# Performance work log

Hardware: AMD Instinct MI355X
Metric: run time of the kernel (lower is better)

Reference implementation:

```python
import jax, jax.numpy as jnp
import numpy as np

DIM = 2048
H = 16       # num_heads
HKV = 4      # num_kv_heads
HD = DIM // H  # head_dim = 128
REP = H // HKV
ROPE_BASE = 10000.0
QK_GAIN_INIT = 1.0
B, T = 4, 2048


def rms_norm(x):
    # F.rms_norm with eps=None -> machine eps of dtype, no weight
    eps = jnp.finfo(x.dtype).eps
    return x * jax.lax.rsqrt(jnp.mean(x * x, axis=-1, keepdims=True) + eps)


def apply_rotary_emb(x, cos, sin):
    # x: [B, h, T, HD]; cos/sin: [T, HD//2]
    h = x.shape[-1] // 2
    x1, x2 = x[..., :h], x[..., h:]
    return jnp.concatenate((x1 * cos + x2 * sin, -x1 * sin + x2 * cos), axis=-1)


def setup_inputs() -> dict:
    key = jax.random.key(0)
    ks = jax.random.split(key, 6)
    kv_dim = HKV * HD
    x = jax.random.normal(ks[0], (B, T, DIM), dtype=jnp.float32)
    Wq = jax.random.normal(ks[1], (DIM, DIM), dtype=jnp.float32) * 0.02
    Wk = jax.random.normal(ks[2], (kv_dim, DIM), dtype=jnp.float32) * 0.02
    Wv = jax.random.normal(ks[3], (kv_dim, DIM), dtype=jnp.float32) * 0.02
    Wproj = jax.random.normal(ks[4], (DIM, DIM), dtype=jnp.float32) * 0.02
    q_gain = jnp.full((H,), QK_GAIN_INIT, dtype=jnp.float32)
    return {"x": x, "Wq": Wq, "Wk": Wk, "Wv": Wv, "Wproj": Wproj, "q_gain": q_gain}


def reference(x, Wq, Wk, Wv, Wproj, q_gain):
    Bs, Ts, D = x.shape
    # QKV projections (bias-free Linear: x @ W.T)
    q = (x @ Wq.T).reshape(Bs, Ts, H, HD).transpose(0, 2, 1, 3)      # [B,H,T,HD]
    k = (x @ Wk.T).reshape(Bs, Ts, HKV, HD).transpose(0, 2, 1, 3)    # [B,HKV,T,HD]
    v = (x @ Wv.T).reshape(Bs, Ts, HKV, HD).transpose(0, 2, 1, 3)
    # RMSNorm over head_dim
    q, k = rms_norm(q), rms_norm(k)
    # rotary
    inv_freq = 1.0 / (ROPE_BASE ** (jnp.arange(0, HD, 2, dtype=jnp.float32) / HD))
    t = jnp.arange(Ts, dtype=jnp.float32)
    freqs = jnp.outer(t, inv_freq)  # [T, HD//2]
    cos, sin = jnp.cos(freqs), jnp.sin(freqs)
    q = apply_rotary_emb(q, cos, sin)
    k = apply_rotary_emb(k, cos, sin)
    # per-head query gain
    q = q * q_gain[None, :, None, None]
    # GQA attention without materializing repeated K/V
    qg = q.reshape(Bs, HKV, REP, Ts, HD)
    scale = 1.0 / jnp.sqrt(jnp.asarray(HD, dtype=q.dtype))
    scores = jnp.einsum('bgrtd,bgsd->bgrts', qg, k) * scale  # [B,HKV,REP,T,T]
    causal = jnp.tril(jnp.ones((Ts, Ts), dtype=bool))
    scores = jnp.where(causal, scores, jnp.finfo(scores.dtype).min)
    attn = jax.nn.softmax(scores, axis=-1)
    y = jnp.einsum('bgrts,bgsd->bgrtd', attn, v)              # [B,HKV,REP,T,HD]
    y = y.reshape(Bs, H, Ts, HD).transpose(0, 2, 1, 3).reshape(Bs, Ts, D)
    return y @ Wproj.T
```

## Files before the change

### kernel.cpp

```cpp
#include <hip/hip_runtime.h>
#include <stdint.h>

typedef unsigned short u16;
typedef __attribute__((ext_vector_type(4))) float f32x4;
typedef __attribute__((ext_vector_type(8))) __bf16 bf16x8;
typedef __attribute__((ext_vector_type(4))) u16 u16x4;
typedef __attribute__((ext_vector_type(8))) u16 u16x8;

#define T_SEQ 2048
#define NB 4
#define NH 16
#define NKV 4
#define HDIM 128
#define PSTR 72

__device__ __forceinline__ u16 f2bf(float f) {
  __bf16 h = (__bf16)f;
  return __builtin_bit_cast(u16, h);
}
__device__ __forceinline__ float bf2f(u16 u) {
  union { uint32_t u; float f; } v; v.u = ((uint32_t)u) << 16;
  return v.f;
}
__device__ __forceinline__ void gload16(const void* g, void* l) {
  __builtin_amdgcn_global_load_lds((const __attribute__((address_space(1))) void*)g,
                                   (__attribute__((address_space(3))) void*)l, 16, 0, 0);
}
__device__ __forceinline__ f32x4 mfma16(bf16x8 a, bf16x8 b, f32x4 c) {
  return __builtin_amdgcn_mfma_f32_16x16x32_bf16(a, b, c, 0, 0, 0);
}

__global__ __launch_bounds__(256) void cvt_all(const float* __restrict__ x,
                                               const float* __restrict__ wq,
                                               const float* __restrict__ wk,
                                               const float* __restrict__ wv,
                                               const float* __restrict__ wp,
                                               u16* __restrict__ xo, u16* __restrict__ wqo,
                                               u16* __restrict__ wko, u16* __restrict__ wvo,
                                               u16* __restrict__ wpo) {
  const int C_X = 16777216 / 4, C_WQ = 4194304 / 4, C_WKV = 1048576 / 4;
  const int B1 = C_X, B2 = B1 + C_WQ, B3 = B2 + C_WKV, B4 = B3 + C_WKV;
  const int total = B4 + C_WQ;
  int idx = blockIdx.x * 256 + threadIdx.x;
  int stride = gridDim.x * 256;
  for (int c = idx; c < total; c += stride) {
    const float* src;
    u16* dst;
    int off;
    if (c < B1)      { src = x;  dst = xo;  off = c; }
    else if (c < B2) { src = wq; dst = wqo; off = c - B1; }
    else if (c < B3) { src = wk; dst = wko; off = c - B2; }
    else if (c < B4) { src = wv; dst = wvo; off = c - B3; }
    else             { src = wp; dst = wpo; off = c - B4; }
    f32x4 v = *(const f32x4*)(src + (size_t)off * 4);
    u16x4 o;
    o[0] = f2bf(v[0]); o[1] = f2bf(v[1]); o[2] = f2bf(v[2]); o[3] = f2bf(v[3]);
    *(u16x4*)(dst + (size_t)off * 4) = o;
  }
}

template <int MODE>
__global__ __launch_bounds__(256) void gemm128p3(const u16* __restrict__ A,
                                                 const u16* __restrict__ Bt,
                                                 u16* __restrict__ k_o, u16* __restrict__ v_o,
                                                 float* __restrict__ f_o,
                                                 int K, int nx, int cpx) {
  __shared__ __align__(16) u16 As3[3 * 128 * 32];
  __shared__ __align__(16) u16 Bs3[3 * 128 * 32];
  const int tid = threadIdx.x;
  const int l = tid & 63, w = tid >> 6;
  const int l15 = l & 15, g16 = l >> 4;
  const int wr = w >> 1, wc = w & 1;

  const int oid = blockIdx.x + nx * blockIdx.y;
  const int wid = (oid & 7) * cpx + (oid >> 3);
  const int m0 = (wid / nx) * 128, n0 = (wid % nx) * 128;

  f32x4 acc[4][4] = {};

  const int row0 = tid >> 2, row1 = 64 + (tid >> 2), cc = tid & 3;
  const int sc0 = cc ^ ((row0 >> 1) & 3), sc1 = cc ^ ((row1 >> 1) & 3);
  const u16* pA0 = A + (size_t)(m0 + row0) * K + sc0 * 8;
  const u16* pA1 = A + (size_t)(m0 + row1) * K + sc1 * 8;
  const u16* pB0 = Bt + (size_t)(n0 + row0) * K + sc0 * 8;
  const u16* pB1 = Bt + (size_t)(n0 + row1) * K + sc1 * 8;

#define STAGE(buf)                                                   \
  {                                                                  \
    char* ab = (char*)As3 + (buf) * 8192 + w * 1024;                 \
    char* bb = (char*)Bs3 + (buf) * 8192 + w * 1024;                 \
    gload16(pA0, ab);                                                \
    gload16(pA1, ab + 4096);                                         \
    gload16(pB0, bb);                                                \
    gload16(pB1, bb + 4096);                                         \
    pA0 += 32; pA1 += 32; pB0 += 32; pB1 += 32;                      \
  }

#define COMPUTE(buf)                                                 \
  {                                                                  \
    const u16* AsB = As3 + (buf) * 4096;                             \
    const u16* BsB = Bs3 + (buf) * 4096;                             \
    bf16x8 af[4], bfr[4];                                            \
    _Pragma("unroll")                                                \
    for (int mt = 0; mt < 4; ++mt) {                                 \
      int arow = wr * 64 + mt * 16 + l15;                            \
      af[mt] = *(const bf16x8*)&AsB[arow * 32 +                      \
                                    ((g16 ^ ((arow >> 1) & 3)) * 8)];\
    }                                                                \
    _Pragma("unroll")                                                \
    for (int nt = 0; nt < 4; ++nt) {                                 \
      int brow = wc * 64 + nt * 16 + l15;                            \
      bfr[nt] = *(const bf16x8*)&BsB[brow * 32 +                     \
                                     ((g16 ^ ((brow >> 1) & 3)) * 8)];\
    }                                                                \
    __builtin_amdgcn_s_setprio(1);                                   \
    _Pragma("unroll")                                                \
    for (int mt = 0; mt < 4; ++mt)                                   \
      _Pragma("unroll")                                              \
      for (int nt = 0; nt < 4; ++nt)                                 \
        acc[mt][nt] = mfma16(af[mt], bfr[nt], acc[mt][nt]);          \
    __builtin_amdgcn_s_setprio(0);                                   \
  }

  const int ntiles = K >> 5;
  STAGE(0);
  STAGE(1);
  asm volatile("s_waitcnt vmcnt(4)" ::: "memory");
  __builtin_amdgcn_s_barrier();

  int cur = 0, nxt = 2;
  for (int t = 0; t < ntiles; ++t) {
    const bool more2 = (t + 2 < ntiles);
    if (more2) STAGE(nxt);
    COMPUTE(cur);
    if (t + 1 < ntiles) {
      if (more2) {
        asm volatile("s_waitcnt vmcnt(4)" ::: "memory");
      } else {
        asm volatile("s_waitcnt vmcnt(0)" ::: "memory");
      }
      __builtin_amdgcn_s_barrier();
    }
    cur = (cur == 2) ? 0 : cur + 1;
    nxt = (nxt == 2) ? 0 : nxt + 1;
  }
#undef STAGE
#undef COMPUTE

#pragma unroll
  for (int mt = 0; mt < 4; ++mt) {
#pragma unroll
    for (int r = 0; r < 4; ++r) {
      int row = m0 + wr * 64 + mt * 16 + g16 * 4 + r;
#pragma unroll
      for (int nt = 0; nt < 4; ++nt) {
        int n = n0 + wc * 64 + nt * 16 + l15;
        float val = acc[mt][nt][r];
        if (MODE == 1) {
          f_o[(size_t)row * 2048 + n] = val;
        } else {
          int b = row >> 11, t = row & (T_SEQ - 1);
          u16 bv = f2bf(val);
          if (n < 512) {
            int h = n >> 7, d = n & 127;
            k_o[((size_t)(b * NKV + h) * T_SEQ + t) * HDIM + d] = bv;
          } else {
            int n2 = n - 512; int h = n2 >> 7, d = n2 & 127;
            v_o[((size_t)(b * NKV + h) * T_SEQ + t) * HDIM + d] = bv;
          }
        }
      }
    }
  }
}

template <int MODE>
__global__ __launch_bounds__(512, 2) void gemm256(const u16* __restrict__ A,
                                                  const u16* __restrict__ Bt,
                                                  u16* __restrict__ q_o,
                                                  float* __restrict__ f_o,
                                                  int K, int ntn, int cpx) {
  __shared__ __align__(16) u16 As[2][256 * 64];
  __shared__ __align__(16) u16 Bs[2][256 * 64];
  const int tid = threadIdx.x;
  const int l = tid & 63, w = tid >> 6;
  const int l16 = l & 15, g16 = l >> 4;
  const int wr = w >> 2, wc = w & 3;

  const int oid = blockIdx.x;
  const int wid = (oid & 7) * cpx + (oid >> 3);
  const int m0 = (wid / ntn) * 256, n0 = (wid % ntn) * 256;

  f32x4 acc[8][4] = {};

  const int srow = tid >> 3, scc = tid & 7;
  const u16* pA[4];
  const u16* pB[4];
#pragma unroll
  for (int j = 0; j < 4; ++j) {
    int row = j * 64 + srow;
    int cc = scc ^ (row & 7);
    pA[j] = A + (size_t)(m0 + row) * K + cc * 8;
    pB[j] = Bt + (size_t)(n0 + row) * K + cc * 8;
  }

#define STAGE(buf)                                              \
  {                                                             \
    char* ab = (char*)As[buf] + w * 1024;                       \
    char* bb = (char*)Bs[buf] + w * 1024;                       \
    _Pragma("unroll")                                           \
    for (int j = 0; j < 4; ++j) {                               \
      gload16(pA[j], ab + j * 8192);                            \
      pA[j] += 64;                                              \
    }                                                           \
    _Pragma("unroll")                                           \
    for (int j = 0; j < 4; ++j) {                               \
      gload16(pB[j], bb + j * 8192);                            \
      pB[j] += 64;                                              \
    }                                                           \
  }

  const int ntk = K >> 6;
  STAGE(0);
  __syncthreads();

  for (int t = 0; t < ntk; ++t) {
    const int buf = t & 1;
    if (t + 1 < ntk) STAGE(buf ^ 1);
#pragma unroll
    for (int ks = 0; ks < 2; ++ks) {
      bf16x8 bfr[4];
#pragma unroll
      for (int nf = 0; nf < 4; ++nf) {
        int brow = wc * 64 + nf * 16 + l16;
        int slot = (ks * 4 + g16) ^ (brow & 7);
        bfr[nf] = *(const bf16x8*)&Bs[buf][brow * 64 + slot * 8];
      }
#pragma unroll
      for (int rh = 0; rh < 2; ++rh) {
        bf16x8 af[4];
#pragma unroll
        for (int f = 0; f < 4; ++f) {
          int arow = wr * 128 + rh * 64 + f * 16 + l16;
          int slot = (ks * 4 + g16) ^ (arow & 7);
          af[f] = *(const bf16x8*)&As[buf][arow * 64 + slot * 8];
        }
        __builtin_amdgcn_s_setprio(1);
#pragma unroll
        for (int f = 0; f < 4; ++f)
#pragma unroll
          for (int nf = 0; nf < 4; ++nf)
            acc[rh * 4 + f][nf] = mfma16(af[f], bfr[nf], acc[rh * 4 + f][nf]);
        __builtin_amdgcn_s_setprio(0);
      }
    }
    __syncthreads();
  }
#undef STAGE

#pragma unroll
  for (int rf = 0; rf < 8; ++rf) {
#pragma unroll
    for (int rr = 0; rr < 4; ++rr) {
      int row = m0 + wr * 128 + rf * 16 + g16 * 4 + rr;
#pragma unroll
      for (int nf = 0; nf < 4; ++nf) {
        int n = n0 + wc * 64 + nf * 16 + l16;
        float val = acc[rf][nf][rr];
        if (MODE == 1) {
          f_o[(size_t)row * 2048 + n] = val;
        } else {
          int b = row >> 11, t = row & (T_SEQ - 1);
          int h = n >> 7, d = n & 127;
          q_o[((size_t)(b * NH + h) * T_SEQ + t) * HDIM + d] = f2bf(val);
        }
      }
    }
  }
}

__global__ __launch_bounds__(256) void postproc(u16* __restrict__ qbuf,
                                                u16* __restrict__ kbuf,
                                                const u16* __restrict__ vbuf,
                                                u16* __restrict__ vtbuf,
                                                const float* __restrict__ gains) {
  const int bid = blockIdx.x;
  if (bid < 40960) {
    const bool isq = (bid < 32768);
    u16* buf = isq ? qbuf : kbuf;
    const int base = isq ? bid : (bid - 32768);
    const int w = threadIdx.x >> 6, l = threadIdx.x & 63;
    const int rid = base * 4 + w;
    const int t = rid & (T_SEQ - 1);
    const int h = (rid >> 11) % (isq ? NH : NKV);
    u16* p = buf + (size_t)rid * HDIM;
    float x1 = bf2f(p[l]), x2 = bf2f(p[l + 64]);
    float ss = x1 * x1 + x2 * x2;
#pragma unroll
    for (int m = 32; m; m >>= 1) ss += __shfl_xor(ss, m, 64);
    float rn = rsqrtf(ss * (1.0f / 128.0f) + 1.1920928955078125e-7f);
    float g = isq ? gains[h] * (1.4426950408889634f / 11.313708498984761f) : 1.0f;
    float sc = rn * g;
    float inv = exp2f(-(float)l * (13.287712379549449f / 64.0f));
    float ang = (float)t * inv;
    float s, c;
    __sincosf(ang, &s, &c);
    float o1 = (x1 * c + x2 * s) * sc;
    float o2 = (x2 * c - x1 * s) * sc;
    p[l] = f2bf(o1);
    p[l + 64] = f2bf(o2);
  } else {
    __shared__ u16 tileT[64][PSTR];
    const int tidx = bid - 40960;
    const int t0 = (tidx & 31) * 64, d0 = ((tidx >> 5) & 1) * 64, bg = tidx >> 6;
    const int tid = threadIdx.x;
    const int row = tid >> 2, c0 = (tid & 3) * 16;
    const u16* src = vbuf + ((size_t)bg * T_SEQ + t0 + row) * HDIM + d0 + c0;
    u16x8 a = *(const u16x8*)src;
    u16x8 bb = *(const u16x8*)(src + 8);
#pragma unroll
    for (int j = 0; j < 8; ++j) {
      tileT[c0 + j][row] = a[j];
      tileT[c0 + 8 + j][row] = bb[j];
    }
    __syncthreads();
    u16* dst = vtbuf + ((size_t)bg * HDIM + d0 + row) * T_SEQ + t0 + c0;
    *(u16x8*)dst = *(const u16x8*)&tileT[row][c0];
    *(u16x8*)(dst + 8) = *(const u16x8*)&tileT[row][c0 + 8];
  }
}

__global__ __launch_bounds__(512) void attn_fwd9(const u16* __restrict__ qb,
                                                 const u16* __restrict__ kb,
                                                 const u16* __restrict__ vtb,
                                                 u16* __restrict__ yb,
                                                 const float* __restrict__ gains) {
  __shared__ __align__(16) u16 Ks[2][64 * 128];
  __shared__ __align__(16) u16 Vs[128 * 64];
  __shared__ __align__(16) u16 Ps[8][16 * PSTR];

  const int tid = threadIdx.x, l = tid & 63, w = tid >> 6;
  const int l16 = l & 15, g16 = l >> 4;

  const int oid = blockIdx.x + 8 * blockIdx.y;
  const int wid = (oid & 7) * 64 + (oid >> 3);
  const int pair = wid & 7, bh = wid >> 3;
  const int b = bh >> 4, h = bh & 15, gr = h >> 2;

  const float Mh = 16.33f * fabsf(gains[h]) + 0.5f;
  const u16* kbase = kb + (size_t)(b * NKV + gr) * T_SEQ * HDIM;
  const u16* vtbase = vtb + (size_t)(b * NKV + gr) * HDIM * T_SEQ;

  bf16x8 ones;
#pragma unroll
  for (int j = 0; j < 8; ++j) ones[j] = (__bf16)1.0f;

  const int krow0 = tid >> 4, kc0 = tid & 15;
  const int krow1 = 32 + (tid >> 4);
  const u16* kp0_base = kbase + (size_t)krow0 * HDIM + (kc0 ^ (krow0 & 7)) * 8;
  const u16* kp1_base = kbase + (size_t)krow1 * HDIM + (kc0 ^ (krow1 & 7)) * 8;
  const int vrow0 = tid >> 3, vc0 = tid & 7;
  const int vrow1 = 64 + (tid >> 3);
  const u16* vp0_base = vtbase + (size_t)vrow0 * T_SEQ + (vc0 ^ (vrow0 & 7)) * 8;
  const u16* vp1_base = vtbase + (size_t)vrow1 * T_SEQ + (vc0 ^ (vrow1 & 7)) * 8;
  char* vd0 = (char*)Vs + (w * 64) * 16;
  char* vd1 = (char*)Vs + (512 + w * 64) * 16;

#define STAGEK(bf)                                                   \
  {                                                                  \
    gload16(kp0, (char*)&Ks[bf][0] + (w * 64) * 16);                 \
    gload16(kp1, (char*)&Ks[bf][0] + ((512 + w * 64)) * 16);         \
    kp0 += 64 * HDIM;                                                \
    kp1 += 64 * HDIM;                                                \
  }
#define STAGEV()                                                     \
  {                                                                  \
    gload16(vp0, vd0);                                               \
    gload16(vp1, vd1);                                               \
    vp0 += 64;                                                       \
    vp1 += 64;                                                       \
  }

#define ATT_TILE(KT, KSBUF)                                                \
  if ((KT) * 64 <= qhi) {                                                  \
    f32x4 sacc[4] = {};                                                    \
    __builtin_amdgcn_s_setprio(1);                                         \
    _Pragma("unroll")                                                      \
    for (int mt = 0; mt < 4; ++mt) {                                       \
      int key = mt * 16 + l16;                                             \
      _Pragma("unroll")                                                    \
      for (int s = 0; s < 4; ++s) {                                        \
        bf16x8 kf = *(const bf16x8*)&Ks[KSBUF][key * 128 +                 \
                                    (((s * 4 + g16) ^ (key & 7)) * 8)];    \
        sacc[mt] = mfma16(kf, qf[s], sacc[mt]);                            \
      }                                                                    \
    }                                                                      \
    __builtin_amdgcn_s_setprio(0);                                         \
    if ((KT) * 64 + 63 > q0) {                                             \
      _Pragma("unroll")                                                    \
      for (int mt = 0; mt < 4; ++mt) {                                     \
        int keyb = (KT) * 64 + mt * 16 + g16 * 4;                          \
        u16x4 p4;                                                          \
        _Pragma("unroll")                                                  \
        for (int r = 0; r < 4; ++r) {                                      \
          float pv = exp2f(sacc[mt][r] - Mh);                              \
          if (keyb + r > q0 + l16) pv = 0.f;                               \
          p4[r] = f2bf(pv);                                                \
        }                                                                  \
        *(u16x4*)&Ps[w][l16 * PSTR + mt * 16 + g16 * 4] = p4;              \
      }                                                                    \
    } else {                                                               \
      _Pragma("unroll")                                                    \
      for (int mt = 0; mt < 4; ++mt) {                                     \
        u16x4 p4;                                                          \
        _Pragma("unroll")                                                  \
        for (int r = 0; r < 4; ++r)                                        \
          p4[r] = f2bf(exp2f(sacc[mt][r] - Mh));                           \
        *(u16x4*)&Ps[w][l16 * PSTR + mt * 16 + g16 * 4] = p4;              \
      }                                                                    \
    }                                                                      \
    __builtin_amdgcn_s_setprio(1);                                         \
    _Pragma("unroll")                                                      \
    for (int ks = 0; ks < 2; ++ks) {                                       \
      bf16x8 pa = *(const bf16x8*)&Ps[w][l16 * PSTR + ks * 32 + g16 * 8];  \
      dden = mfma16(pa, ones, dden);                                       \
      _Pragma("unroll")                                                    \
      for (int dt = 0; dt < 8; ++dt) {                                     \
        int d = dt * 16 + l16;                                             \
        bf16x8 vv = *(const bf16x8*)&Vs[d * 64 +                           \
                                    (((ks * 4 + g16) ^ (d & 7)) * 8)];     \
        oacc[dt] = mfma16(pa, vv, oacc[dt]);                               \
      }                                                                    \
    }                                                                      \
    __builtin_amdgcn_s_setprio(0);                                         \
  }

  for (int phase = 0; phase < 2; ++phase) {
    const int qt = phase ? (15 - pair) : pair;
    const int q0 = qt * 128 + w * 16;
    const int qhi = q0 + 15;

    bf16x8 qf[4];
    const u16* qbase = qb + ((size_t)bh * T_SEQ + q0) * HDIM;
#pragma unroll
    for (int s = 0; s < 4; ++s)
      qf[s] = *(const bf16x8*)(qbase + (size_t)l16 * HDIM + s * 32 + g16 * 8);

    f32x4 oacc[8] = {};
    f32x4 dden = {};
    const int ntile = 2 * qt + 2;

    const u16* kp0 = kp0_base;
    const u16* kp1 = kp1_base;
    const u16* vp0 = vp0_base;
    const u16* vp1 = vp1_base;

    STAGEK(0);
    STAGEV();

    for (int kt = 0; kt < ntile; kt += 2) {
      STAGEK(1);
      asm volatile("s_waitcnt vmcnt(2)" ::: "memory");
      __builtin_amdgcn_s_barrier();
      ATT_TILE(kt, 0);
      __builtin_amdgcn_s_barrier();
      STAGEV();

      const bool more = (kt + 2 < ntile);
      if (more) STAGEK(0);
      if (more) {
        asm volatile("s_waitcnt vmcnt(2)" ::: "memory");
      } else {
        asm volatile("s_waitcnt vmcnt(0)" ::: "memory");
      }
      __builtin_amdgcn_s_barrier();
      ATT_TILE(kt + 1, 1);
      __builtin_amdgcn_s_barrier();
      if (more) STAGEV();
    }

    float rden[4];
#pragma unroll
    for (int r = 0; r < 4; ++r) rden[r] = 1.f / dden[r];

#pragma unroll
    for (int dt = 0; dt < 8; ++dt)
#pragma unroll
      for (int r = 0; r < 4; ++r) {
        int t = q0 + g16 * 4 + r;
        int d = dt * 16 + l16;
        yb[(((size_t)b * T_SEQ + t) * NH + h) * HDIM + d] = f2bf(oacc[dt][r] * rden[r]);
      }
    __syncthreads();
  }
#undef STAGEK
#undef STAGEV
#undef ATT_TILE
}

extern "C" void kernel_launch(void* const* d_in, const int* in_sizes, int n_in,
                              void* d_out, int out_size, void* d_ws, size_t ws_size,
                              hipStream_t stream) {
  const float* x = (const float*)d_in[0];
  const float* Wq = (const float*)d_in[1];
  const float* Wk = (const float*)d_in[2];
  const float* Wv = (const float*)d_in[3];
  const float* Wproj = (const float*)d_in[4];
  const float* qg = (const float*)d_in[5];
  float* out = (float*)d_out;

  u16* xbf = (u16*)d_ws;
  u16* Wqkv = xbf + (size_t)8192 * 2048;
  u16* Wpj = Wqkv + (size_t)3072 * 2048;
  u16* qbuf = Wpj + (size_t)2048 * 2048;
  u16* kbuf = qbuf + (size_t)8192 * 2048;
  u16* vbuf = kbuf + (size_t)2048 * 2048;
  u16* ybuf = xbf;
  u16* vtbuf = Wqkv;

  cvt_all<<<2048, 256, 0, stream>>>(x, Wq, Wk, Wv, Wproj,
                                    xbf, Wqkv, Wqkv + (size_t)2048 * 2048,
                                    Wqkv + (size_t)2560 * 2048, Wpj);

  gemm256<0><<<256, 512, 0, stream>>>(xbf, Wqkv, qbuf, nullptr, 2048, 8, 32);

  gemm128p3<2><<<dim3(8, 64), 256, 0, stream>>>(xbf, Wqkv + (size_t)2048 * 2048,
                                                kbuf, vbuf, nullptr, 2048, 8, 64);

  postproc<<<41984, 256, 0, stream>>>(qbuf, kbuf, vbuf, vtbuf, qg);

  attn_fwd9<<<dim3(8, 64), 512, 0, stream>>>(qbuf, kbuf, vtbuf, ybuf, qg);

  gemm256<1><<<256, 512, 0, stream>>>(ybuf, Wpj, nullptr, out, 2048, 8, 32);
}
```

Before: 361.5 us.

## Process both paired query tiles in one pass sharing each K/V tile load

The attention kernel now handles its two causal-paired query tiles together in a single loop over key tiles. Each K/V tile is loaded once and used by both query sets, where before the two phases each streamed the keys separately. This removes the duplicated K/V traffic of the shorter tile. The K double buffer and software pipelining are replaced by a single-buffered load followed by a sync, and the P scratch uses an XOR swizzle instead of padding. The cost is roughly double the accumulator registers, exposed load latency without prefetch, and a launch-bounds hint asking for higher occupancy that may force spills.

After: 446.5 us. 1.24x slower.

```diff
diff --git a/kernel.cpp b/kernel.cpp
--- a/kernel.cpp
+++ b/kernel.cpp
@@ -330,17 +330,18 @@
   }
 }
 
-__global__ __launch_bounds__(512) void attn_fwd9(const u16* __restrict__ qb,
-                                                 const u16* __restrict__ kb,
-                                                 const u16* __restrict__ vtb,
-                                                 u16* __restrict__ yb,
-                                                 const float* __restrict__ gains) {
-  __shared__ __align__(16) u16 Ks[2][64 * 128];
+__global__ __launch_bounds__(512, 4) void attn_fwd11(const u16* __restrict__ qb,
+                                                     const u16* __restrict__ kb,
+                                                     const u16* __restrict__ vtb,
+                                                     u16* __restrict__ yb,
+                                                     const float* __restrict__ gains) {
+  __shared__ __align__(16) u16 Ks[64 * 128];
   __shared__ __align__(16) u16 Vs[128 * 64];
-  __shared__ __align__(16) u16 Ps[8][16 * PSTR];
+  __shared__ __align__(16) u16 Ps[8][16 * 64];
 
   const int tid = threadIdx.x, l = tid & 63, w = tid >> 6;
   const int l16 = l & 15, g16 = l >> 4;
+  const int pswz = (l16 & 7) * 8;
 
   const int oid = blockIdx.x + 8 * blockIdx.y;
   const int wid = (oid & 7) * 64 + (oid >> 3);
@@ -357,32 +358,38 @@
 
   const int krow0 = tid >> 4, kc0 = tid & 15;
   const int krow1 = 32 + (tid >> 4);
-  const u16* kp0_base = kbase + (size_t)krow0 * HDIM + (kc0 ^ (krow0 & 7)) * 8;
-  const u16* kp1_base = kbase + (size_t)krow1 * HDIM + (kc0 ^ (krow1 & 7)) * 8;
+  const u16* kp0 = kbase + (size_t)krow0 * HDIM + (kc0 ^ (krow0 & 7)) * 8;
+  const u16* kp1 = kbase + (size_t)krow1 * HDIM + (kc0 ^ (krow1 & 7)) * 8;
   const int vrow0 = tid >> 3, vc0 = tid & 7;
   const int vrow1 = 64 + (tid >> 3);
-  const u16* vp0_base = vtbase + (size_t)vrow0 * T_SEQ + (vc0 ^ (vrow0 & 7)) * 8;
-  const u16* vp1_base = vtbase + (size_t)vrow1 * T_SEQ + (vc0 ^ (vrow1 & 7)) * 8;
+  const u16* vp0 = vtbase + (size_t)vrow0 * T_SEQ + (vc0 ^ (vrow0 & 7)) * 8;
+  const u16* vp1 = vtbase + (size_t)vrow1 * T_SEQ + (vc0 ^ (vrow1 & 7)) * 8;
+  char* kd0 = (char*)Ks + (w * 64) * 16;
+  char* kd1 = (char*)Ks + (512 + w * 64) * 16;
   char* vd0 = (char*)Vs + (w * 64) * 16;
   char* vd1 = (char*)Vs + (512 + w * 64) * 16;
 
-#define STAGEK(bf)                                                   \
-  {                                                                  \
-    gload16(kp0, (char*)&Ks[bf][0] + (w * 64) * 16);                 \
-    gload16(kp1, (char*)&Ks[bf][0] + ((512 + w * 64)) * 16);         \
-    kp0 += 64 * HDIM;                                                \
-    kp1 += 64 * HDIM;                                                \
-  }
-#define STAGEV()                                                     \
-  {                                                                  \
-    gload16(vp0, vd0);                                               \
-    gload16(vp1, vd1);                                               \
-    vp0 += 64;                                                       \
-    vp1 += 64;                                                       \
-  }
-
-#define ATT_TILE(KT, KSBUF)                                                \
-  if ((KT) * 64 <= qhi) {                                                  \
+  const int q0a = pair * 128 + w * 16;
+  const int q0b = (15 - pair) * 128 + w * 16;
+  const int qhia = q0a + 15;
+
+  bf16x8 qfa[4], qfb[4];
+  {
+    const u16* qba = qb + ((size_t)bh * T_SEQ + q0a) * HDIM;
+    const u16* qbb = qb + ((size_t)bh * T_SEQ + q0b) * HDIM;
+#pragma unroll
+    for (int s = 0; s < 4; ++s) {
+      qfa[s] = *(const bf16x8*)(qba + (size_t)l16 * HDIM + s * 32 + g16 * 8);
+      qfb[s] = *(const bf16x8*)(qbb + (size_t)l16 * HDIM + s * 32 + g16 * 8);
+    }
+  }
+
+  f32x4 oacca[8] = {}, oaccb[8] = {};
+  f32x4 ddena = {}, ddenb = {};
+  const int ntb = 2 * (15 - pair) + 2;
+
+#define ATT_SET(KT, QF, Q0, OACC, DDEN)                                    \
+  {                                                                        \
     f32x4 sacc[4] = {};                                                    \
     __builtin_amdgcn_s_setprio(1);                                         \
     _Pragma("unroll")                                                      \
@@ -390,13 +397,13 @@
       int key = mt * 16 + l16;                                             \
       _Pragma("unroll")                                                    \
       for (int s = 0; s < 4; ++s) {                                        \
-        bf16x8 kf = *(const bf16x8*)&Ks[KSBUF][key * 128 +                 \
+        bf16x8 kf = *(const bf16x8*)&Ks[key * 128 +                        \
                                     (((s * 4 + g16) ^ (key & 7)) * 8)];    \
-        sacc[mt] = mfma16(kf, qf[s], sacc[mt]);                            \
+        sacc[mt] = mfma16(kf, QF[s], sacc[mt]);                            \
       }                                                                    \
     }                                                                      \
     __builtin_amdgcn_s_setprio(0);                                         \
-    if ((KT) * 64 + 63 > q0) {                                             \
+    if ((KT) * 64 + 63 > (Q0)) {                                           \
       _Pragma("unroll")                                                    \
       for (int mt = 0; mt < 4; ++mt) {                                     \
         int keyb = (KT) * 64 + mt * 16 + g16 * 4;                          \
@@ -404,10 +411,10 @@
         _Pragma("unroll")                                                  \
         for (int r = 0; r < 4; ++r) {                                      \
           float pv = exp2f(sacc[mt][r] - Mh);                              \
-          if (keyb + r > q0 + l16) pv = 0.f;                               \
+          if (keyb + r > (Q0) + l16) pv = 0.f;                             \
           p4[r] = f2bf(pv);                                                \
         }                                                                  \
-        *(u16x4*)&Ps[w][l16 * PSTR + mt * 16 + g16 * 4] = p4;              \
+        *(u16x4*)&Ps[w][l16 * 64 + ((mt * 16 + g16 * 4) ^ pswz)] = p4;     \
       }                                                                    \
     } else {                                                               \
       _Pragma("unroll")                                                    \
@@ -416,86 +423,57 @@
         _Pragma("unroll")                                                  \
         for (int r = 0; r < 4; ++r)                                        \
           p4[r] = f2bf(exp2f(sacc[mt][r] - Mh));                           \
-        *(u16x4*)&Ps[w][l16 * PSTR + mt * 16 + g16 * 4] = p4;              \
+        *(u16x4*)&Ps[w][l16 * 64 + ((mt * 16 + g16 * 4) ^ pswz)] = p4;     \
       }                                                                    \
     }                                                                      \
     __builtin_amdgcn_s_setprio(1);                                         \
     _Pragma("unroll")                                                      \
     for (int ks = 0; ks < 2; ++ks) {                                       \
-      bf16x8 pa = *(const bf16x8*)&Ps[w][l16 * PSTR + ks * 32 + g16 * 8];  \
-      dden = mfma16(pa, ones, dden);                                       \
+      bf16x8 pa = *(const bf16x8*)&Ps[w][l16 * 64 +                        \
+                                         ((ks * 32 + g16 * 8) ^ pswz)];    \
+      DDEN = mfma16(pa, ones, DDEN);                                       \
       _Pragma("unroll")                                                    \
       for (int dt = 0; dt < 8; ++dt) {                                     \
         int d = dt * 16 + l16;                                             \
         bf16x8 vv = *(const bf16x8*)&Vs[d * 64 +                           \
                                     (((ks * 4 + g16) ^ (d & 7)) * 8)];     \
-        oacc[dt] = mfma16(pa, vv, oacc[dt]);                               \
+        OACC[dt] = mfma16(pa, vv, OACC[dt]);                               \
       }                                                                    \
     }                                                                      \
     __builtin_amdgcn_s_setprio(0);                                         \
   }
 
-  for (int phase = 0; phase < 2; ++phase) {
-    const int qt = phase ? (15 - pair) : pair;
-    const int q0 = qt * 128 + w * 16;
-    const int qhi = q0 + 15;
-
-    bf16x8 qf[4];
-    const u16* qbase = qb + ((size_t)bh * T_SEQ + q0) * HDIM;
-#pragma unroll
-    for (int s = 0; s < 4; ++s)
-      qf[s] = *(const bf16x8*)(qbase + (size_t)l16 * HDIM + s * 32 + g16 * 8);
-
-    f32x4 oacc[8] = {};
-    f32x4 dden = {};
-    const int ntile = 2 * qt + 2;
-
-    const u16* kp0 = kp0_base;
-    const u16* kp1 = kp1_base;
-    const u16* vp0 = vp0_base;
-    const u16* vp1 = vp1_base;
-
-    STAGEK(0);
-    STAGEV();
-
-    for (int kt = 0; kt < ntile; kt += 2) {
-      STAGEK(1);
-      asm volatile("s_waitcnt vmcnt(2)" ::: "memory");
-      __builtin_amdgcn_s_barrier();
-      ATT_TILE(kt, 0);
-      __builtin_amdgcn_s_barrier();
-      STAGEV();
-
-      const bool more = (kt + 2 < ntile);
-      if (more) STAGEK(0);
-      if (more) {
-        asm volatile("s_waitcnt vmcnt(2)" ::: "memory");
-      } else {
-        asm volatile("s_waitcnt vmcnt(0)" ::: "memory");
-      }
-      __builtin_amdgcn_s_barrier();
-      ATT_TILE(kt + 1, 1);
-      __builtin_amdgcn_s_barrier();
-      if (more) STAGEV();
-    }
-
-    float rden[4];
-#pragma unroll
-    for (int r = 0; r < 4; ++r) rden[r] = 1.f / dden[r];
-
-#pragma unroll
-    for (int dt = 0; dt < 8; ++dt)
-#pragma unroll
-      for (int r = 0; r < 4; ++r) {
-        int t = q0 + g16 * 4 + r;
-        int d = dt * 16 + l16;
-        yb[(((size_t)b * T_SEQ + t) * NH + h) * HDIM + d] = f2bf(oacc[dt][r] * rden[r]);
-      }
+  for (int kt = 0; kt < ntb; ++kt) {
+    gload16(kp0, kd0);
+    gload16(kp1, kd1);
+    gload16(vp0, vd0);
+    gload16(vp1, vd1);
+    kp0 += 64 * HDIM; kp1 += 64 * HDIM;
+    vp0 += 64; vp1 += 64;
     __syncthreads();
-  }
-#undef STAGEK
-#undef STAGEV
-#undef ATT_TILE
+
+    if (kt * 64 <= qhia) ATT_SET(kt, qfa, q0a, oacca, ddena);
+    ATT_SET(kt, qfb, q0b, oaccb, ddenb);
+    __syncthreads();
+  }
+#undef ATT_SET
+
+  float rdena[4], rdenb[4];
+#pragma unroll
+  for (int r = 0; r < 4; ++r) {
+    rdena[r] = 1.f / ddena[r];
+    rdenb[r] = 1.f / ddenb[r];
+  }
+#pragma unroll
+  for (int dt = 0; dt < 8; ++dt)
+#pragma unroll
+    for (int r = 0; r < 4; ++r) {
+      int d = dt * 16 + l16;
+      int ta = q0a + g16 * 4 + r;
+      int tb = q0b + g16 * 4 + r;
+      yb[(((size_t)b * T_SEQ + ta) * NH + h) * HDIM + d] = f2bf(oacca[dt][r] * rdena[r]);
+      yb[(((size_t)b * T_SEQ + tb) * NH + h) * HDIM + d] = f2bf(oaccb[dt][r] * rdenb[r]);
+    }
 }
 
 extern "C" void kernel_launch(void* const* d_in, const int* in_sizes, int n_in,
@@ -529,7 +507,7 @@
 
   postproc<<<41984, 256, 0, stream>>>(qbuf, kbuf, vbuf, vtbuf, qg);
 
-  attn_fwd9<<<dim3(8, 64), 512, 0, stream>>>(qbuf, kbuf, vtbuf, ybuf, qg);
+  attn_fwd11<<<dim3(8, 64), 512, 0, stream>>>(qbuf, kbuf, vtbuf, ybuf, qg);
 
   gemm256<1><<<256, 512, 0, stream>>>(ybuf, Wpj, nullptr, out, 2048, 8, 32);
 }
```
